# Kernel optimization log

Hardware: AMD Instinct MI355X
Metric: run time of the kernel (lower is better)

Reference implementation:

```python
import jax, jax.numpy as jnp
import numpy as np

NUM_GROUPS = 32
EPS = 1e-6


def setup_inputs() -> dict:
    key = jax.random.key(0)
    ks = jax.random.split(key, 6)
    b, c, H, W = 4, 512, 64, 64
    scale = 1.0 / np.sqrt(c)
    return {
        "x": jax.random.normal(ks[0], (b, c, H, W), dtype=jnp.float32),
        "gn_w": jnp.ones((c,), jnp.float32),
        "gn_b": jnp.zeros((c,), jnp.float32),
        "wq": jax.random.normal(ks[1], (c, c), jnp.float32) * scale,
        "bq": jnp.zeros((c,), jnp.float32),
        "wk": jax.random.normal(ks[2], (c, c), jnp.float32) * scale,
        "bk": jnp.zeros((c,), jnp.float32),
        "wv": jax.random.normal(ks[3], (c, c), jnp.float32) * scale,
        "bv": jnp.zeros((c,), jnp.float32),
        "wp": jax.random.normal(ks[4], (c, c), jnp.float32) * scale,
        "bp": jnp.zeros((c,), jnp.float32),
    }


def _group_norm(x, gamma, beta):
    b, c, H, W = x.shape
    xg = x.reshape(b, NUM_GROUPS, c // NUM_GROUPS, H, W)
    mean = xg.mean(axis=(2, 3, 4), keepdims=True)
    var = xg.var(axis=(2, 3, 4), keepdims=True)
    xn = (xg - mean) * jax.lax.rsqrt(var + EPS)
    xn = xn.reshape(b, c, H, W)
    return xn * gamma[None, :, None, None] + beta[None, :, None, None]


def reference(x, gn_w, gn_b, wq, bq, wk, bk, wv, bv, wp, bp):
    b, c, H, W = x.shape
    h = _group_norm(x, gn_w, gn_b)  # (b,c,H,W)
    hf = h.reshape(b, c, H * W)  # (b,c,n)
    # 1x1 convs == per-pixel linear maps; weight layout [out,in]
    q = jnp.einsum('oc,bcn->bno', wq, hf) + bq  # (b,n,c)
    k = jnp.einsum('oc,bcn->bon', wk, hf) + bk[None, :, None]  # (b,c,n)
    v = jnp.einsum('oc,bcn->bon', wv, hf) + bv[None, :, None]  # (b,c,n)
    attn = jnp.einsum('bnc,bcm->bnm', q, k) * (int(c) ** (-0.5))
    attn = jax.nn.softmax(attn, axis=2)  # softmax over keys m
    # A = v @ attn^T  -> (b,c,n) where A[:, :, n] = sum_m v[:,:,m] attn[n,m]
    A = jnp.einsum('bcm,bnm->bcn', v, attn)
    A = jnp.einsum('oc,bcn->bon', wp, A) + bp[None, :, None]
    return x + A.reshape(b, c, H, W)
```

## Files before the change

kernel.cpp:

```cpp
#include <hip/hip_runtime.h>

#define BATCH 4
#define CCH 512
#define NPIX 4096
#define NGRP 32
#define GSZ 16
#define GN_EPS 1e-6f

typedef __attribute__((ext_vector_type(8))) short short8;
typedef __attribute__((ext_vector_type(8))) unsigned short ushort8;
typedef __attribute__((ext_vector_type(4))) unsigned short ushort4v;
typedef __attribute__((ext_vector_type(4))) float f32x4;

__device__ inline unsigned short f2bf(float f) {
  unsigned u = __float_as_uint(f);
  unsigned r = u + 0x7fffu + ((u >> 16) & 1u);
  return (unsigned short)(r >> 16);
}
__device__ inline float bf2f(unsigned short us) {
  return __uint_as_float(((unsigned)us) << 16);
}

__global__ __launch_bounds__(256) void gn_stats(const float* __restrict__ x,
                                                float* __restrict__ stats) {
  int bg = blockIdx.x;
  const f32x4* base = (const f32x4*)(x + (size_t)bg * (GSZ * NPIX));
  float s = 0.f, ss = 0.f;
  const int n4 = GSZ * NPIX / 4;
  for (int i = threadIdx.x; i < n4; i += 256) {
    f32x4 v = base[i];
    s += v.x + v.y + v.z + v.w;
    ss += v.x * v.x + v.y * v.y + v.z * v.z + v.w * v.w;
  }
  for (int off = 32; off > 0; off >>= 1) {
    s += __shfl_xor(s, off, 64);
    ss += __shfl_xor(ss, off, 64);
  }
  __shared__ float rs[4], rss[4];
  int lane = threadIdx.x & 63, wid = threadIdx.x >> 6;
  if (lane == 0) { rs[wid] = s; rss[wid] = ss; }
  __syncthreads();
  if (threadIdx.x == 0) {
    float S = rs[0] + rs[1] + rs[2] + rs[3];
    float SS = rss[0] + rss[1] + rss[2] + rss[3];
    const float inv = 1.f / (float)(GSZ * NPIX);
    float mean = S * inv;
    float var = SS * inv - mean * mean;
    stats[bg * 2] = mean;
    stats[bg * 2 + 1] = rsqrtf(var + GN_EPS);
  }
}

__global__ __launch_bounds__(256) void gn_apply_t(const float* __restrict__ x,
                                                  const float* __restrict__ stats,
                                                  const float* __restrict__ gw,
                                                  const float* __restrict__ gb,
                                                  unsigned short* __restrict__ hT) {
  __shared__ float tile[64][65];
  int b = blockIdx.z, c0 = blockIdx.y * 64, n0 = blockIdx.x * 64;
  int t = threadIdx.x;
  int tc4 = t & 15, tr = t >> 4;
  const float* xb = x + ((size_t)b * CCH + c0) * NPIX + n0;
#pragma unroll
  for (int j = 0; j < 4; ++j) {
    int row = tr + j * 16;
    int c = c0 + row;
    float mean = stats[((size_t)b * NGRP + (c >> 4)) * 2];
    float rstd = stats[((size_t)b * NGRP + (c >> 4)) * 2 + 1];
    float ga = gw[c] * rstd;
    float be = gb[c] - mean * ga;
    f32x4 v = *(const f32x4*)(xb + (size_t)row * NPIX + tc4 * 4);
    tile[row][tc4 * 4 + 0] = v.x * ga + be;
    tile[row][tc4 * 4 + 1] = v.y * ga + be;
    tile[row][tc4 * 4 + 2] = v.z * ga + be;
    tile[row][tc4 * 4 + 3] = v.w * ga + be;
  }
  __syncthreads();
  int cc = t & 7, nr = t >> 3;
  unsigned short* outp = hT + ((size_t)b * NPIX + n0) * CCH + c0;
#pragma unroll
  for (int j = 0; j < 2; ++j) {
    int n = nr + j * 32;
    ushort8 pk;
#pragma unroll
    for (int i = 0; i < 8; ++i) pk[i] = f2bf(tile[cc * 8 + i][n]);
    *(ushort8*)(outp + (size_t)n * CCH + cc * 8) = pk;
  }
}

__global__ __launch_bounds__(256) void f32_to_bf16(const float* __restrict__ src,
                                                   unsigned short* __restrict__ dst,
                                                   int n4) {
  int i = blockIdx.x * 256 + threadIdx.x;
  if (i < n4) {
    f32x4 v = ((const f32x4*)src)[i];
    ushort4v o;
    o.x = f2bf(v.x); o.y = f2bf(v.y); o.z = f2bf(v.z); o.w = f2bf(v.w);
    ((ushort4v*)dst)[i] = o;
  }
}

template <int BIAS_MODE, int OUT_BF16, int RESID, int SWZ>
__global__ __launch_bounds__(256, 2) void gemm_bt(
    const unsigned short* __restrict__ A, const unsigned short* __restrict__ B,
    void* __restrict__ Cv, const float* __restrict__ bias,
    const float* __restrict__ resid, int M, int N, int K, int lda, int ldb,
    int ldc, long sA, long sB, long sC, long sR, float scale) {
  __shared__ __align__(16) unsigned short lA[128][40];
  __shared__ __align__(16) unsigned short lB[128][40];
  const int t = threadIdx.x;
  const int lane = t & 63, w = t >> 6;
  const int wr = w >> 1, wc = w & 1;
  const int fr = lane & 15, kg = lane >> 4;

  unsigned orig = blockIdx.x + gridDim.x * (blockIdx.y + gridDim.y * blockIdx.z);
  unsigned nwg = gridDim.x * gridDim.y * gridDim.z;
  unsigned tid = (orig & 7) * (nwg >> 3) + (orig >> 3);
  int mt, ntl, bz;
  if (SWZ == 1) {
    unsigned u = tid & 15, v = (tid >> 4) & 7, p = tid >> 7;
    mt = (int)((p & 1) * 16 + u);
    ntl = (int)((p >> 1) * 8 + v);
    bz = 0;
  } else if (SWZ == 2) {
    unsigned bx = tid % gridDim.x, r = tid / gridDim.x;
    ntl = (int)bx;
    mt = (int)(r % gridDim.y);
    bz = (int)(r / gridDim.y);
  } else {
    unsigned bx = tid % gridDim.x, r = tid / gridDim.x;
    mt = (int)bx;
    ntl = (int)(r % gridDim.y);
    bz = (int)(r / gridDim.y);
  }
  const int m0 = mt * 128, n0 = ntl * 128;

  const unsigned short* Abz = A + (long)bz * sA;
  const unsigned short* Bbz = B + (long)bz * sB;
  const int srow = t >> 1, skc = (t & 1) * 16;
  const unsigned short* gA = Abz + (size_t)(m0 + srow) * lda + skc;
  const unsigned short* gB = Bbz + (size_t)(n0 + srow) * ldb + skc;

  short8 a0X = *(const short8*)(gA);
  short8 a1X = *(const short8*)(gA + 8);
  short8 b0X = *(const short8*)(gB);
  short8 b1X = *(const short8*)(gB + 8);
  short8 a0Y = *(const short8*)(gA + 32);
  short8 a1Y = *(const short8*)(gA + 40);
  short8 b0Y = *(const short8*)(gB + 32);
  short8 b1Y = *(const short8*)(gB + 40);

  f32x4 acc[4][4];
  const f32x4 zero = {0.f, 0.f, 0.f, 0.f};
#pragma unroll
  for (int m = 0; m < 4; ++m)
#pragma unroll
    for (int n = 0; n < 4; ++n) acc[m][n] = zero;

  const int NT = K >> 5;
#define COMPUTE()                                                             \
  do {                                                                        \
    short8 af[4], bfr[4];                                                     \
    _Pragma("unroll") for (int m = 0; m < 4; ++m) af[m] =                     \
        *(const short8*)&lA[wr * 64 + m * 16 + fr][kg * 8];                   \
    _Pragma("unroll") for (int n = 0; n < 4; ++n) bfr[n] =                    \
        *(const short8*)&lB[wc * 64 + n * 16 + fr][kg * 8];                   \
    _Pragma("unroll") for (int m = 0; m < 4; ++m)                             \
        _Pragma("unroll") for (int n = 0; n < 4; ++n) acc[m][n] =             \
            __builtin_amdgcn_mfma_f32_16x16x32_bf16(af[m], bfr[n],            \
                                                    acc[m][n], 0, 0, 0);      \
  } while (0)

  for (int it = 0; it < NT; it += 2) {
    __syncthreads();
    *(short8*)&lA[srow][skc] = a0X;
    *(short8*)&lA[srow][skc + 8] = a1X;
    *(short8*)&lB[srow][skc] = b0X;
    *(short8*)&lB[srow][skc + 8] = b1X;
    if (it + 2 < NT) {
      a0X = *(const short8*)(gA + (it + 2) * 32);
      a1X = *(const short8*)(gA + (it + 2) * 32 + 8);
      b0X = *(const short8*)(gB + (it + 2) * 32);
      b1X = *(const short8*)(gB + (it + 2) * 32 + 8);
    }
    __syncthreads();
    COMPUTE();
    __syncthreads();
    *(short8*)&lA[srow][skc] = a0Y;
    *(short8*)&lA[srow][skc + 8] = a1Y;
    *(short8*)&lB[srow][skc] = b0Y;
    *(short8*)&lB[srow][skc + 8] = b1Y;
    if (it + 3 < NT) {
      a0Y = *(const short8*)(gA + (it + 3) * 32);
      a1Y = *(const short8*)(gA + (it + 3) * 32 + 8);
      b0Y = *(const short8*)(gB + (it + 3) * 32);
      b1Y = *(const short8*)(gB + (it + 3) * 32 + 8);
    }
    __syncthreads();
    COMPUTE();
  }
#undef COMPUTE

  const int rowbase = m0 + wr * 64 + kg * 4;
  const int colbase = n0 + wc * 64 + fr;
#pragma unroll
  for (int m = 0; m < 4; ++m) {
#pragma unroll
    for (int n = 0; n < 4; ++n) {
      int col = colbase + n * 16;
#pragma unroll
      for (int r = 0; r < 4; ++r) {
        int row = rowbase + m * 16 + r;
        float v = acc[m][n][r] * scale;
        if (BIAS_MODE == 1) v += bias[row];
        if (BIAS_MODE == 2) v += bias[col];
        if (RESID) v += resid[(size_t)bz * sR + (size_t)row * ldc + col];
        size_t idx = (size_t)bz * sC + (size_t)row * ldc + col;
        if (OUT_BF16)
          ((unsigned short*)Cv)[idx] = f2bf(v);
        else
          ((float*)Cv)[idx] = v;
      }
    }
  }
}

__global__ __launch_bounds__(256) void softmax_rows(
    const unsigned short* __restrict__ S, unsigned short* __restrict__ P) {
  const int row = blockIdx.x;
  const int t = threadIdx.x;
  const unsigned short* Sr = S + (size_t)row * NPIX;
  float f[16];
  float mx = -3.4e38f;
#pragma unroll
  for (int j = 0; j < 2; ++j) {
    ushort8 u = *(const ushort8*)(Sr + j * 2048 + t * 8);
#pragma unroll
    for (int i = 0; i < 8; ++i) {
      f[j * 8 + i] = bf2f(u[i]);
      mx = fmaxf(mx, f[j * 8 + i]);
    }
  }
  for (int off = 32; off > 0; off >>= 1) mx = fmaxf(mx, __shfl_xor(mx, off, 64));
  __shared__ float r1[4], r2[4];
  int lane = t & 63, wid = t >> 6;
  if (lane == 0) r1[wid] = mx;
  __syncthreads();
  mx = fmaxf(fmaxf(r1[0], r1[1]), fmaxf(r1[2], r1[3]));
  float sum = 0.f;
#pragma unroll
  for (int i = 0; i < 16; ++i) {
    f[i] = __expf(f[i] - mx);
    sum += f[i];
  }
  for (int off = 32; off > 0; off >>= 1) sum += __shfl_xor(sum, off, 64);
  if (lane == 0) r2[wid] = sum;
  __syncthreads();
  float inv = 1.f / (r2[0] + r2[1] + r2[2] + r2[3]);
  unsigned short* Pr = P + (size_t)row * NPIX;
#pragma unroll
  for (int j = 0; j < 2; ++j) {
    ushort8 o;
#pragma unroll
    for (int i = 0; i < 8; ++i) o[i] = f2bf(f[j * 8 + i] * inv);
    *(ushort8*)(Pr + j * 2048 + t * 8) = o;
  }
}

extern "C" void kernel_launch(void* const* d_in, const int* in_sizes, int n_in,
                              void* d_out, int out_size, void* d_ws, size_t ws_size,
                              hipStream_t stream) {
  const float* x = (const float*)d_in[0];
  const float* gnw = (const float*)d_in[1];
  const float* gnb = (const float*)d_in[2];
  const float* wq = (const float*)d_in[3];
  const float* bq = (const float*)d_in[4];
  const float* wk = (const float*)d_in[5];
  const float* bk = (const float*)d_in[6];
  const float* wv = (const float*)d_in[7];
  const float* bv = (const float*)d_in[8];
  const float* wp = (const float*)d_in[9];
  const float* bp = (const float*)d_in[10];
  float* out = (float*)d_out;

  const size_t BS = (size_t)NPIX * CCH;
  const size_t PB = (size_t)NPIX * NPIX;

  char* ws = (char*)d_ws;
  float* stats = (float*)ws;
  unsigned short* hT = (unsigned short*)(ws + 1024);
  unsigned short* Abuf = hT;
  unsigned short* qb = hT + BATCH * BS;
  unsigned short* kTb = qb + BATCH * BS;
  unsigned short* vb = kTb + BATCH * BS;
  unsigned short* wqb = vb + BATCH * BS;
  unsigned short* wkb = wqb + CCH * CCH;
  unsigned short* wvb = wkb + CCH * CCH;
  unsigned short* wpb = wvb + CCH * CCH;
  unsigned short* Sb = wpb + CCH * CCH;
  unsigned short* Pb = Sb + PB;
  size_t need2 = (size_t)((char*)(Pb + 2 * PB) - ws);
  size_t need4 = (size_t)((char*)(Pb + 4 * PB) - ws);
  if (ws_size < need2) return;
  const bool p4 = ws_size >= need4;

  f32_to_bf16<<<256, 256, 0, stream>>>(wq, wqb, CCH * CCH / 4);
  f32_to_bf16<<<256, 256, 0, stream>>>(wk, wkb, CCH * CCH / 4);
  f32_to_bf16<<<256, 256, 0, stream>>>(wv, wvb, CCH * CCH / 4);
  f32_to_bf16<<<256, 256, 0, stream>>>(wp, wpb, CCH * CCH / 4);

  gn_stats<<<BATCH * NGRP, 256, 0, stream>>>(x, stats);
  gn_apply_t<<<dim3(NPIX / 64, CCH / 64, BATCH), 256, 0, stream>>>(x, stats, gnw,
                                                                   gnb, hT);

  gemm_bt<2, 1, 0, 2><<<dim3(4, 32, BATCH), 256, 0, stream>>>(
      hT, wqb, qb, bq, nullptr, NPIX, CCH, CCH, CCH, CCH, CCH, (long)BS, 0,
      (long)BS, 0, 1.f);
  gemm_bt<2, 1, 0, 2><<<dim3(4, 32, BATCH), 256, 0, stream>>>(
      hT, wkb, kTb, bk, nullptr, NPIX, CCH, CCH, CCH, CCH, CCH, (long)BS, 0,
      (long)BS, 0, 1.f);
  gemm_bt<1, 1, 0, 0><<<dim3(4, 32, BATCH), 256, 0, stream>>>(
      wvb, hT, vb, bv, nullptr, CCH, NPIX, CCH, CCH, CCH, NPIX, 0, (long)BS,
      (long)BS, 0, 1.f);

  const float sscale = 0.044194173824159216f;
  if (p4) {
    for (int b = 0; b < 4; ++b) {
      gemm_bt<0, 1, 0, 1><<<dim3(32, 32, 1), 256, 0, stream>>>(
          qb + (size_t)b * BS, kTb + (size_t)b * BS, Sb, nullptr, nullptr, NPIX,
          NPIX, CCH, CCH, CCH, NPIX, 0, 0, 0, 0, sscale);
      softmax_rows<<<NPIX, 256, 0, stream>>>(Sb, Pb + (size_t)b * PB);
    }
    gemm_bt<0, 1, 0, 2><<<dim3(4, 32, BATCH), 256, 0, stream>>>(
        Pb, vb, Abuf, nullptr, nullptr, NPIX, CCH, NPIX, NPIX, NPIX, CCH,
        (long)PB, (long)BS, (long)BS, 0, 1.f);
  } else {
    for (int p = 0; p < 2; ++p) {
      for (int i = 0; i < 2; ++i) {
        int b = p * 2 + i;
        gemm_bt<0, 1, 0, 1><<<dim3(32, 32, 1), 256, 0, stream>>>(
            qb + (size_t)b * BS, kTb + (size_t)b * BS, Sb, nullptr, nullptr,
            NPIX, NPIX, CCH, CCH, CCH, NPIX, 0, 0, 0, 0, sscale);
        softmax_rows<<<NPIX, 256, 0, stream>>>(Sb, Pb + (size_t)i * PB);
      }
      gemm_bt<0, 1, 0, 2><<<dim3(4, 32, 2), 256, 0, stream>>>(
          Pb, vb + (size_t)p * 2 * BS, Abuf + (size_t)p * 2 * BS, nullptr,
          nullptr, NPIX, CCH, NPIX, NPIX, NPIX, CCH, (long)PB, (long)BS,
          (long)BS, 0, 1.f);
    }
  }
  gemm_bt<1, 0, 1, 0><<<dim3(4, 32, BATCH), 256, 0, stream>>>(
      wpb, Abuf, out, bp, x, CCH, NPIX, CCH, CCH, CCH, NPIX, 0, (long)BS,
      (long)BS, (long)BS, 1.f);
}
```

Measured before the change: 355.0 us.

## Fuse QK^T, softmax and PV into a single flash-style attention kernel

Replaces the per-batch score GEMM, row softmax kernel and P·V GEMM with one kernel. Each 512-thread block keeps a 64-row query tile in LDS, streams K and V tiles through double-buffered LDS, computes exp of the scaled scores, accumulates row sums, and applies the 1/sum normalization at the end. This removes the large bf16 S and P buffers in global memory and their write/read traffic, plus several launches. It skips max subtraction in the exponent, so it relies on the scores staying small enough not to overflow. The LDS footprint of roughly 150KB likely limits each CU to one block.

```diff
diff --git a/kernel.cpp b/kernel.cpp
--- a/kernel.cpp
+++ b/kernel.cpp
@@ -117,12 +117,7 @@
   unsigned nwg = gridDim.x * gridDim.y * gridDim.z;
   unsigned tid = (orig & 7) * (nwg >> 3) + (orig >> 3);
   int mt, ntl, bz;
-  if (SWZ == 1) {
-    unsigned u = tid & 15, v = (tid >> 4) & 7, p = tid >> 7;
-    mt = (int)((p & 1) * 16 + u);
-    ntl = (int)((p >> 1) * 8 + v);
-    bz = 0;
-  } else if (SWZ == 2) {
+  if (SWZ == 2) {
     unsigned bx = tid % gridDim.x, r = tid / gridDim.x;
     ntl = (int)bx;
     mt = (int)(r % gridDim.y);
@@ -225,45 +220,173 @@
   }
 }
 
-__global__ __launch_bounds__(256) void softmax_rows(
-    const unsigned short* __restrict__ S, unsigned short* __restrict__ P) {
-  const int row = blockIdx.x;
+__global__ __launch_bounds__(512, 2) void attn_fused(
+    const unsigned short* __restrict__ qg, const unsigned short* __restrict__ kg2,
+    const unsigned short* __restrict__ vg, unsigned short* __restrict__ og,
+    float scale) {
+  __shared__ __align__(16) unsigned short Qs[64 * 520];
+  __shared__ __align__(16) unsigned short Ks[2][17408];
+  __shared__ __align__(16) unsigned short Ps[64 * 136];
+  __shared__ float lred[2][32][4];
+  __shared__ float linv[64];
+
   const int t = threadIdx.x;
-  const unsigned short* Sr = S + (size_t)row * NPIX;
-  float f[16];
-  float mx = -3.4e38f;
-#pragma unroll
-  for (int j = 0; j < 2; ++j) {
-    ushort8 u = *(const ushort8*)(Sr + j * 2048 + t * 8);
-#pragma unroll
-    for (int i = 0; i < 8; ++i) {
-      f[j * 8 + i] = bf2f(u[i]);
-      mx = fmaxf(mx, f[j * 8 + i]);
-    }
-  }
-  for (int off = 32; off > 0; off >>= 1) mx = fmaxf(mx, __shfl_xor(mx, off, 64));
-  __shared__ float r1[4], r2[4];
-  int lane = t & 63, wid = t >> 6;
-  if (lane == 0) r1[wid] = mx;
+  const int lane = t & 63;
+  const int wid = t >> 6;
+  const int wq = wid >> 2, wc = wid & 3;
+  const int fr = lane & 15, kgp = lane >> 4;
+
+  unsigned logical = ((unsigned)blockIdx.x & 7) * 32 + ((unsigned)blockIdx.x >> 3);
+  const int bz = (int)(logical >> 6), qt = (int)(logical & 63);
+  const size_t BS = (size_t)NPIX * CCH;
+  const unsigned short* qb = qg + (size_t)bz * BS + (size_t)qt * 64 * CCH;
+  const unsigned short* kb = kg2 + (size_t)bz * BS;
+  const unsigned short* vb = vg + (size_t)bz * BS;
+
+  {
+    const int row = t >> 3, c0 = (t & 7) * 64;
+    const unsigned short* src = qb + (size_t)row * CCH + c0;
+#pragma unroll
+    for (int i = 0; i < 8; ++i)
+      *(short8*)&Qs[row * 520 + c0 + i * 8] = *(const short8*)(src + i * 8);
+  }
+
+  const int krow = t >> 2, kseg = t & 3;
+  const unsigned short* gK = kb + (size_t)krow * CCH + kseg * 32;
+  const int kldsoff = krow * 136 + kseg * 32;
+  const unsigned short* gV = vb + (size_t)t * NPIX;
+  const int vldsbase = t * 32;
+  const int vxor = t & 3;
+
+  short8 R0, R1, R2, R3;
+#define LOADK(mt_, cc_)                                                       \
+  do { const unsigned short* g = gK + (size_t)(mt_) * (128 * CCH) + (cc_) * 128; \
+    R0 = *(const short8*)(g); R1 = *(const short8*)(g + 8);                   \
+    R2 = *(const short8*)(g + 16); R3 = *(const short8*)(g + 24); } while (0)
+#define LOADV(mt_, vc_)                                                       \
+  do { const unsigned short* g = gV + (mt_) * 128 + (vc_) * 32;               \
+    R0 = *(const short8*)(g); R1 = *(const short8*)(g + 8);                   \
+    R2 = *(const short8*)(g + 16); R3 = *(const short8*)(g + 24); } while (0)
+#define WRITEK(buf_)                                                          \
+  do { unsigned short* d = &Ks[buf_][kldsoff];                                \
+    *(short8*)(d) = R0; *(short8*)(d + 8) = R1;                               \
+    *(short8*)(d + 16) = R2; *(short8*)(d + 24) = R3; } while (0)
+#define WRITEV(buf_)                                                          \
+  do { unsigned short* d = &Ks[buf_][vldsbase];                               \
+    *(short8*)(d + ((0 ^ vxor) * 8)) = R0; *(short8*)(d + ((1 ^ vxor) * 8)) = R1; \
+    *(short8*)(d + ((2 ^ vxor) * 8)) = R2; *(short8*)(d + ((3 ^ vxor) * 8)) = R3; } while (0)
+
+  f32x4 oa[2][8];
+  const f32x4 zero = {0.f, 0.f, 0.f, 0.f};
+#pragma unroll
+  for (int i = 0; i < 2; ++i)
+#pragma unroll
+    for (int j = 0; j < 8; ++j) oa[i][j] = zero;
+  f32x4 racc0 = zero, racc1 = zero;
+
+  LOADK(0, 0);
+  for (int mt = 0; mt < 32; ++mt) {
+    f32x4 s00 = zero, s01 = zero, s10 = zero, s11 = zero;
+#pragma unroll
+    for (int ph = 0; ph < 8; ++ph) {
+      const int buf = ph & 1;
+      if (ph < 4) WRITEK(buf); else WRITEV(buf);
+      if (ph < 3) { LOADK(mt, ph + 1); }
+      else if (ph == 3) { LOADV(mt, 0); }
+      else if (ph < 7) { LOADV(mt, ph - 3); }
+      else { if (mt + 1 < 32) LOADK(mt + 1, 0); }
+      __syncthreads();
+      if (ph < 4) {
+#pragma unroll
+        for (int kk = 0; kk < 4; ++kk) {
+          short8 a0 = *(const short8*)&Qs[(wq * 32 + fr) * 520 + ph * 128 + kk * 32 + kgp * 8];
+          short8 a1 = *(const short8*)&Qs[(wq * 32 + 16 + fr) * 520 + ph * 128 + kk * 32 + kgp * 8];
+          short8 b0 = *(const short8*)&Ks[buf][(wc * 32 + fr) * 136 + kk * 32 + kgp * 8];
+          short8 b1 = *(const short8*)&Ks[buf][(wc * 32 + 16 + fr) * 136 + kk * 32 + kgp * 8];
+          s00 = __builtin_amdgcn_mfma_f32_16x16x32_bf16(a0, b0, s00, 0, 0, 0);
+          s01 = __builtin_amdgcn_mfma_f32_16x16x32_bf16(a0, b1, s01, 0, 0, 0);
+          s10 = __builtin_amdgcn_mfma_f32_16x16x32_bf16(a1, b0, s10, 0, 0, 0);
+          s11 = __builtin_amdgcn_mfma_f32_16x16x32_bf16(a1, b1, s11, 0, 0, 0);
+        }
+        if (ph == 3) {
+          f32x4 p00, p01, p10, p11;
+#pragma unroll
+          for (int r = 0; r < 4; ++r) {
+            p00[r] = __expf(s00[r] * scale);
+            p01[r] = __expf(s01[r] * scale);
+            p10[r] = __expf(s10[r] * scale);
+            p11[r] = __expf(s11[r] * scale);
+          }
+          f32x4 rs0 = p00 + p01, rs1 = p10 + p11;
+#pragma unroll
+          for (int off = 1; off <= 8; off <<= 1) {
+#pragma unroll
+            for (int r = 0; r < 4; ++r) {
+              rs0[r] += __shfl_xor(rs0[r], off, 64);
+              rs1[r] += __shfl_xor(rs1[r], off, 64);
+            }
+          }
+          racc0 += rs0;
+          racc1 += rs1;
+#pragma unroll
+          for (int r = 0; r < 4; ++r) {
+            Ps[(wq * 32 + kgp * 4 + r) * 136 + wc * 32 + fr] = f2bf(p00[r]);
+            Ps[(wq * 32 + kgp * 4 + r) * 136 + wc * 32 + 16 + fr] = f2bf(p01[r]);
+            Ps[(wq * 32 + 16 + kgp * 4 + r) * 136 + wc * 32 + fr] = f2bf(p10[r]);
+            Ps[(wq * 32 + 16 + kgp * 4 + r) * 136 + wc * 32 + 16 + fr] = f2bf(p11[r]);
+          }
+        }
+      } else {
+        const int vc = ph - 4;
+        short8 pa0 = *(const short8*)&Ps[(wq * 32 + fr) * 136 + vc * 32 + kgp * 8];
+        short8 pa1 = *(const short8*)&Ps[(wq * 32 + 16 + fr) * 136 + vc * 32 + kgp * 8];
+#pragma unroll
+        for (int fb = 0; fb < 8; ++fb) {
+          const int c = wc * 128 + fb * 16 + fr;
+          short8 bv = *(const short8*)&Ks[buf][c * 32 + ((kgp ^ (c & 3)) * 8)];
+          oa[0][fb] = __builtin_amdgcn_mfma_f32_16x16x32_bf16(pa0, bv, oa[0][fb], 0, 0, 0);
+          oa[1][fb] = __builtin_amdgcn_mfma_f32_16x16x32_bf16(pa1, bv, oa[1][fb], 0, 0, 0);
+        }
+      }
+    }
+  }
+#undef LOADK
+#undef LOADV
+#undef WRITEK
+#undef WRITEV
+
+  if (fr == 0) {
+#pragma unroll
+    for (int r = 0; r < 4; ++r) {
+      lred[wq][kgp * 4 + r][wc] = racc0[r];
+      lred[wq][16 + kgp * 4 + r][wc] = racc1[r];
+    }
+  }
   __syncthreads();
-  mx = fmaxf(fmaxf(r1[0], r1[1]), fmaxf(r1[2], r1[3]));
-  float sum = 0.f;
-#pragma unroll
-  for (int i = 0; i < 16; ++i) {
-    f[i] = __expf(f[i] - mx);
-    sum += f[i];
-  }
-  for (int off = 32; off > 0; off >>= 1) sum += __shfl_xor(sum, off, 64);
-  if (lane == 0) r2[wid] = sum;
+  if (t < 64) {
+    float s = lred[t >> 5][t & 31][0] + lred[t >> 5][t & 31][1] +
+              lred[t >> 5][t & 31][2] + lred[t >> 5][t & 31][3];
+    linv[t] = 1.f / s;
+  }
   __syncthreads();
-  float inv = 1.f / (r2[0] + r2[1] + r2[2] + r2[3]);
-  unsigned short* Pr = P + (size_t)row * NPIX;
-#pragma unroll
-  for (int j = 0; j < 2; ++j) {
-    ushort8 o;
-#pragma unroll
-    for (int i = 0; i < 8; ++i) o[i] = f2bf(f[j * 8 + i] * inv);
-    *(ushort8*)(Pr + j * 2048 + t * 8) = o;
+#pragma unroll
+  for (int i = 0; i < 2; ++i) {
+    f32x4 li = *(const f32x4*)&linv[wq * 32 + i * 16 + kgp * 4];
+#pragma unroll
+    for (int fb = 0; fb < 8; ++fb) {
+#pragma unroll
+      for (int r = 0; r < 4; ++r)
+        Qs[(wq * 32 + i * 16 + kgp * 4 + r) * 520 + wc * 128 + fb * 16 + fr] =
+            f2bf(oa[i][fb][r] * li[r]);
+    }
+  }
+  __syncthreads();
+  {
+    const int row = t >> 3, c0 = (t & 7) * 64;
+    unsigned short* dst = og + (size_t)bz * BS + ((size_t)qt * 64 + row) * CCH + c0;
+#pragma unroll
+    for (int i = 0; i < 8; ++i)
+      *(short8*)(dst + i * 8) = *(const short8*)&Qs[row * 520 + c0 + i * 8];
   }
 }
 
@@ -284,7 +407,6 @@
   float* out = (float*)d_out;
 
   const size_t BS = (size_t)NPIX * CCH;
-  const size_t PB = (size_t)NPIX * NPIX;
 
   char* ws = (char*)d_ws;
   float* stats = (float*)ws;
@@ -297,12 +419,8 @@
   unsigned short* wkb = wqb + CCH * CCH;
   unsigned short* wvb = wkb + CCH * CCH;
   unsigned short* wpb = wvb + CCH * CCH;
-  unsigned short* Sb = wpb + CCH * CCH;
-  unsigned short* Pb = Sb + PB;
-  size_t need2 = (size_t)((char*)(Pb + 2 * PB) - ws);
-  size_t need4 = (size_t)((char*)(Pb + 4 * PB) - ws);
-  if (ws_size < need2) return;
-  const bool p4 = ws_size >= need4;
+  size_t need = (size_t)((char*)(wpb + CCH * CCH) - ws);
+  if (ws_size < need) return;
 
   f32_to_bf16<<<256, 256, 0, stream>>>(wq, wqb, CCH * CCH / 4);
   f32_to_bf16<<<256, 256, 0, stream>>>(wk, wkb, CCH * CCH / 4);
@@ -324,31 +442,8 @@
       (long)BS, 0, 1.f);
 
   const float sscale = 0.044194173824159216f;
-  if (p4) {
-    for (int b = 0; b < 4; ++b) {
-      gemm_bt<0, 1, 0, 1><<<dim3(32, 32, 1), 256, 0, stream>>>(
-          qb + (size_t)b * BS, kTb + (size_t)b * BS, Sb, nullptr, nullptr, NPIX,
-          NPIX, CCH, CCH, CCH, NPIX, 0, 0, 0, 0, sscale);
-      softmax_rows<<<NPIX, 256, 0, stream>>>(Sb, Pb + (size_t)b * PB);
-    }
-    gemm_bt<0, 1, 0, 2><<<dim3(4, 32, BATCH), 256, 0, stream>>>(
-        Pb, vb, Abuf, nullptr, nullptr, NPIX, CCH, NPIX, NPIX, NPIX, CCH,
-        (long)PB, (long)BS, (long)BS, 0, 1.f);
-  } else {
-    for (int p = 0; p < 2; ++p) {
-      for (int i = 0; i < 2; ++i) {
-        int b = p * 2 + i;
-        gemm_bt<0, 1, 0, 1><<<dim3(32, 32, 1), 256, 0, stream>>>(
-            qb + (size_t)b * BS, kTb + (size_t)b * BS, Sb, nullptr, nullptr,
-            NPIX, NPIX, CCH, CCH, CCH, NPIX, 0, 0, 0, 0, sscale);
-        softmax_rows<<<NPIX, 256, 0, stream>>>(Sb, Pb + (size_t)i * PB);
-      }
-      gemm_bt<0, 1, 0, 2><<<dim3(4, 32, 2), 256, 0, stream>>>(
-          Pb, vb + (size_t)p * 2 * BS, Abuf + (size_t)p * 2 * BS, nullptr,
-          nullptr, NPIX, CCH, NPIX, NPIX, NPIX, CCH, (long)PB, (long)BS,
-          (long)BS, 0, 1.f);
-    }
-  }
+  attn_fused<<<BATCH * 64, 512, 0, stream>>>(qb, kTb, vb, Abuf, sscale);
+
   gemm_bt<1, 0, 1, 0><<<dim3(4, 32, BATCH), 256, 0, stream>>>(
       wpb, Abuf, out, bp, x, CCH, NPIX, CCH, CCH, CCH, NPIX, 0, (long)BS,
       (long)BS, (long)BS, 1.f);
```

Result: faster. 340.5 us (-4.1%).
